# Optimization experiments

Hardware: AMD Instinct MI355X
Metric: run time of the kernel (lower is better)

## Reference

```python
import jax, jax.numpy as jnp
import numpy as np

N_NODES = 50000
N_EDGES = 1600000
IN_FEATS = 256
HIDDEN = 128
N_CLASSES = 40


def setup_inputs() -> dict:
    key = jax.random.key(0)
    k1, k2, k3, k4, k5, k6 = jax.random.split(key, 6)
    inputs = jax.random.normal(k1, (N_NODES, IN_FEATS), dtype=jnp.float32)
    src = jax.random.randint(k2, (N_EDGES,), 0, N_NODES, dtype=jnp.int64 if jax.config.jax_enable_x64 else jnp.int32)
    dst = jax.random.randint(k3, (N_EDGES,), 0, N_NODES, dtype=jnp.int64 if jax.config.jax_enable_x64 else jnp.int32)
    # glorot-style init for GraphConv weights, zero bias (DGL defaults)
    W1 = jax.random.normal(k4, (IN_FEATS, HIDDEN), dtype=jnp.float32) * (1.0 / np.sqrt(IN_FEATS))
    b1 = jnp.zeros((HIDDEN,), dtype=jnp.float32)
    W2 = jax.random.normal(k5, (HIDDEN, N_CLASSES), dtype=jnp.float32) * (1.0 / np.sqrt(HIDDEN))
    b2 = jnp.zeros((N_CLASSES,), dtype=jnp.float32)
    return {"inputs": inputs, "src": src, "dst": dst, "W1": W1, "b1": b1, "W2": W2, "b2": b2}


def _graph_conv(x, W, b, src, dst, deg_out_isqrt, deg_in_isqrt):
    # DGL GraphConv, norm='both': D_dst^{-1/2} A (D_src^{-1/2} X W) + b
    # W applied before aggregation (in_feats >= out_feats path)
    h = (x * deg_out_isqrt[:, None]) @ W                      # [N, out]
    msg = h[src]                                              # [E, out] gather
    agg = jax.ops.segment_sum(msg, dst, num_segments=x.shape[0])  # [N, out] scatter-add
    return agg * deg_in_isqrt[:, None] + b


def reference(inputs, src, dst, W1, b1, W2, b2):
    n = inputs.shape[0]
    ones = jnp.ones((src.shape[0],), dtype=inputs.dtype)
    deg_out = jax.ops.segment_sum(ones, src, num_segments=n)
    deg_in = jax.ops.segment_sum(ones, dst, num_segments=n)
    deg_out_isqrt = jnp.where(deg_out > 0, jax.lax.rsqrt(jnp.maximum(deg_out, 1.0)), 0.0)
    deg_in_isqrt = jnp.where(deg_in > 0, jax.lax.rsqrt(jnp.maximum(deg_in, 1.0)), 0.0)
    h = _graph_conv(inputs, W1, b1, src, dst, deg_out_isqrt, deg_in_isqrt)
    h = _graph_conv(h, W2, b2, src, dst, deg_out_isqrt, deg_in_isqrt)
    return jax.nn.log_softmax(h, axis=1)
```

## Files before the change

### kernel.cpp

```cpp
#include <hip/hip_runtime.h>
#include <math.h>

#define N_NODES 50000
#define N_EDGES 1600000
#define IN_F 256
#define HID 128
#define NCLS 40
#define HS2 40
#define NP 50048
#define NBINS 196
#define MS_BLOCKS 200
#define MS_CHUNK 8000
#define BC_BLOCKS 400
#define BC_CHUNK 4000
#define BIN_CAP 12288

typedef __attribute__((ext_vector_type(8))) short short8;
typedef __attribute__((ext_vector_type(4))) float v4f;
typedef __attribute__((ext_vector_type(2))) _Float16 h2v;

__device__ __forceinline__ unsigned short f2bf(float f) {
    union { float f; unsigned int i; } v;
    v.f = f;
    unsigned int r = v.i + 0x7FFF + ((v.i >> 16) & 1);
    return (unsigned short)(r >> 16);
}
__device__ __forceinline__ h2v u2h(unsigned int u) {
    union { unsigned int i; h2v h; } v; v.i = u; return v.h;
}
__device__ __forceinline__ unsigned int h2u(h2v h) {
    union { h2v h; unsigned int i; } v; v.h = h; return v.i;
}


__global__ __launch_bounds__(256) void k_zero(int* __restrict__ hist_g) {
    for (int i = threadIdx.x; i < 2 * NBINS; i += 256) hist_g[i] = 0;
}


__global__ __launch_bounds__(256) void k_big(const int* __restrict__ src,
                                             const int* __restrict__ dst,
                                             int* __restrict__ hist_g,
                                             const float* __restrict__ W1,
                                             const float* __restrict__ b1,
                                             const float* __restrict__ W2,
                                             short* __restrict__ w12f,
                                             float* __restrict__ b1w2) {
    __shared__ int smem[HID * NCLS];
    int t = threadIdx.x;
    if (blockIdx.x < BC_BLOCKS) {
        int* h = smem;
        for (int i = t; i < 2 * NBINS; i += 256) h[i] = 0;
        __syncthreads();
        int e0 = blockIdx.x * BC_CHUNK;
        for (int i = t * 4; i < BC_CHUNK; i += 1024) {
            int4 d4 = *(const int4*)&dst[e0 + i];
            int4 s4 = *(const int4*)&src[e0 + i];
            atomicAdd(&h[d4.x >> 8], 1);
            atomicAdd(&h[d4.y >> 8], 1);
            atomicAdd(&h[d4.z >> 8], 1);
            atomicAdd(&h[d4.w >> 8], 1);
            atomicAdd(&h[NBINS + (s4.x >> 8)], 1);
            atomicAdd(&h[NBINS + (s4.y >> 8)], 1);
            atomicAdd(&h[NBINS + (s4.z >> 8)], 1);
            atomicAdd(&h[NBINS + (s4.w >> 8)], 1);
        }
        __syncthreads();
        for (int i = t; i < 2 * NBINS; i += 256)
            if (h[i]) atomicAdd(&hist_g[i], h[i]);
        return;
    }
    if (blockIdx.x == BC_BLOCKS + 6) {
        int c = t;
        if (c < NCLS) {
            float a0 = 0.f, a1 = 0.f, a2 = 0.f, a3 = 0.f;
            for (int k = 0; k < HID; k += 4) {
                a0 += b1[k + 0] * W2[(k + 0) * NCLS + c];
                a1 += b1[k + 1] * W2[(k + 1) * NCLS + c];
                a2 += b1[k + 2] * W2[(k + 2) * NCLS + c];
                a3 += b1[k + 3] * W2[(k + 3) * NCLS + c];
            }
            b1w2[c] = (a0 + a1) + (a2 + a3);
        }
        return;
    }
    float* w2s = (float*)smem;
    for (int i = t; i < HID * NCLS; i += 256) w2s[i] = W2[i];
    __syncthreads();
    int g = (blockIdx.x - BC_BLOCKS) * 256 + t;
    int kt = g / 192, rem = g % 192;
    int nt = rem >> 6, lane = rem & 63;
    int q = lane >> 4, n = lane & 15;
    int col = nt * 16 + n;
    float acc[8];
#pragma unroll
    for (int j = 0; j < 8; j++) acc[j] = 0.f;
    if (col < NCLS) {
        int k0 = kt * 32 + q * 8;
        const float* w1r = &W1[(size_t)k0 * HID];
        for (int jj = 0; jj < HID; jj += 4) {
            float w0 = w2s[(jj + 0) * NCLS + col];
            float w1v = w2s[(jj + 1) * NCLS + col];
            float w2v = w2s[(jj + 2) * NCLS + col];
            float w3 = w2s[(jj + 3) * NCLS + col];
#pragma unroll
            for (int j = 0; j < 8; j++) {
                float4 a = *(const float4*)&w1r[j * HID + jj];
                acc[j] += a.x * w0 + a.y * w1v + a.z * w2v + a.w * w3;
            }
        }
    }
    short8 v;
#pragma unroll
    for (int j = 0; j < 8; j++) v[j] = (short)f2bf(acc[j]);
    *(short8*)&w12f[(size_t)g * 8] = v;
}

__global__ __launch_bounds__(256) void k_binscan(const int* __restrict__ hist_g,
                                                 int* __restrict__ bo_d, int* __restrict__ bo_s,
                                                 int* __restrict__ cur_d, int* __restrict__ cur_s) {
    __shared__ int sm[256];
    int t = threadIdx.x;
    for (int side = 0; side < 2; side++) {
        int v = (t < NBINS) ? hist_g[side * NBINS + t] : 0;
        sm[t] = v;
        __syncthreads();
        for (int off = 1; off < 256; off <<= 1) {
            int a = (t >= off) ? sm[t - off] : 0;
            __syncthreads();
            sm[t] += a;
            __syncthreads();
        }
        int ex = sm[t] - v;
        int* bo = side ? bo_s : bo_d;
        int* cu = side ? cur_s : cur_d;
        if (t < NBINS) { bo[t] = ex; cu[t] = ex; }
        if (t == 0) bo[NBINS] = N_EDGES;
        __syncthreads();
    }
}

__global__ __launch_bounds__(256) void k_msscatter(const int* __restrict__ src,
                                                   const int* __restrict__ dst,
                                                   int* __restrict__ cur_d, int* __restrict__ cur_s,
                                                   int* __restrict__ binned_d,
                                                   unsigned char* __restrict__ binned_s) {
    __shared__ int hist[NBINS];
    __shared__ int delta[NBINS];
    __shared__ int lcur[NBINS];
    __shared__ int sm[256];
    __shared__ int stage[MS_CHUNK];
    __shared__ unsigned char binof[MS_CHUNK];
    int t = threadIdx.x;
    int side = blockIdx.x / MS_BLOCKS;
    int e0 = (blockIdx.x % MS_BLOCKS) * MS_CHUNK;
    const int* key = side ? src : dst;
    for (int i = t; i < NBINS; i += 256) hist[i] = 0;
    __syncthreads();
    for (int i = t; i < MS_CHUNK; i += 256) atomicAdd(&hist[key[e0 + i] >> 8], 1);
    __syncthreads();
    int hv = (t < NBINS) ? hist[t] : 0;
    sm[t] = hv;
    __syncthreads();
    for (int off = 1; off < 256; off <<= 1) {
        int a = (t >= off) ? sm[t - off] : 0;
        __syncthreads();
        sm[t] += a;
        __syncthreads();
    }
    if (t < NBINS) {
        int ex = sm[t] - hv;
        int g = atomicAdd(side ? &cur_s[t] : &cur_d[t], hv);
        delta[t] = g - ex;
        lcur[t] = ex;
    }
    __syncthreads();
    if (side == 0) {
        for (int i = t; i < MS_CHUNK; i += 256) {
            int kf = key[e0 + i];
            int v = src[e0 + i];
            int b = kf >> 8;
            int pos = atomicAdd(&lcur[b], 1);
            stage[pos] = ((kf & 255) << 16) | v;
            binof[pos] = (unsigned char)b;
        }
        __syncthreads();
        for (int i = t; i < MS_CHUNK; i += 256)
            binned_d[i + delta[binof[i]]] = stage[i];
    } else {
        for (int i = t; i < MS_CHUNK; i += 256) {
            int kf = key[e0 + i];
            int b = kf >> 8;
            int pos = atomicAdd(&lcur[b], 1);
            stage[pos] = kf & 255;
            binof[pos] = (unsigned char)b;
        }
        __syncthreads();
        for (int i = t; i < MS_CHUNK; i += 256)
            binned_s[i + delta[binof[i]]] = (unsigned char)stage[i];
    }
}

__global__ __launch_bounds__(256) void k_bins(const int* __restrict__ binned_d,
                                              const unsigned char* __restrict__ binned_s,
                                              const int* __restrict__ bo_d, const int* __restrict__ bo_s,
                                              int* __restrict__ offsets, float* __restrict__ din,
                                              float* __restrict__ dout,
                                              unsigned short* __restrict__ csr16) {
    __shared__ int hist[256];
    __shared__ int sm[256];
    __shared__ int cur[256];
    __shared__ int stage[BIN_CAP];
    int t = threadIdx.x;
    hist[t] = 0;
    __syncthreads();
    if (blockIdx.x < NBINS) {
        int bin = blockIdx.x;
        int beg = bo_d[bin], end = bo_d[bin + 1];
        int n = end - beg;
        for (int i = t; i < n; i += 256) atomicAdd(&hist[binned_d[beg + i] >> 16], 1);
        __syncthreads();
        int hv = hist[t];
        sm[t] = hv;
        __syncthreads();
        for (int off = 1; off < 256; off <<= 1) {
            int a = (t >= off) ? sm[t - off] : 0;
            __syncthreads();
            sm[t] += a;
            __syncthreads();
        }
        int ex = sm[t] - hv;
        int node = bin * 256 + t;
        if (node < N_NODES) {
            offsets[node] = beg + ex;
            din[node] = hv ? rsqrtf((float)hv) : 0.f;
        }
        cur[t] = ex;
        __syncthreads();
        for (int i = t; i < n; i += 256) {
            int p = binned_d[beg + i];
            int pos = atomicAdd(&cur[p >> 16], 1);
            if (pos < BIN_CAP) stage[pos] = p & 0xFFFF;
        }
        __syncthreads();
        int m = n < BIN_CAP ? n : BIN_CAP;
        for (int i = t; i < m; i += 256) csr16[beg + i] = (unsigned short)stage[i];
    } else {
        int bin = blockIdx.x - NBINS;
        int beg = bo_s[bin], end = bo_s[bin + 1];
        for (int i = t; i < end - beg; i += 256) atomicAdd(&hist[binned_s[beg + i]], 1);
        __syncthreads();
        int node = bin * 256 + t;
        if (node < N_NODES) {
            int hv2 = hist[t];
            dout[node] = hv2 ? rsqrtf((float)hv2) : 0.f;
        }
    }
}


__global__ __launch_bounds__(256) void k_gemm1(const float* __restrict__ x,
                                               const short* __restrict__ w12f,
                                               const float* __restrict__ dout,
                                               _Float16* __restrict__ gt) {
    int t = threadIdx.x;
    int wv = t >> 6, lane = t & 63;
    int q = lane >> 4, lr = lane & 15;
    int m0 = blockIdx.x * 64 + wv * 16;
    int row = m0 + lr;
    int rowc = min(row, N_NODES - 1);
    v4f acc[3];
#pragma unroll
    for (int n = 0; n < 3; n++) acc[n] = (v4f){0.f, 0.f, 0.f, 0.f};

    const float* xr = &x[(size_t)rowc * IN_F];
#pragma unroll
    for (int kt = 0; kt < 8; kt++) {
        const float4* ap = (const float4*)&xr[kt * 32 + q * 8];
        float4 a0 = ap[0], a1 = ap[1];
        short8 af;
        af[0] = (short)f2bf(a0.x); af[1] = (short)f2bf(a0.y);
        af[2] = (short)f2bf(a0.z); af[3] = (short)f2bf(a0.w);
        af[4] = (short)f2bf(a1.x); af[5] = (short)f2bf(a1.y);
        af[6] = (short)f2bf(a1.z); af[7] = (short)f2bf(a1.w);
#pragma unroll
        for (int nt = 0; nt < 3; nt++) {
            short8 bf = *(const short8*)&w12f[(size_t)((kt * 3 + nt) * 64 + lane) * 8];
            acc[nt] = __builtin_amdgcn_mfma_f32_16x16x32_bf16(af, bf, acc[nt], 0, 0, 0);
        }
    }
    int rbase = m0 + q * 4;
    float4 dv = *(const float4*)&dout[rbase];
#pragma unroll
    for (int i = 0; i < 4; i++) {
        int orow = rbase + i;
        if (orow < N_NODES) {
            float s = (i == 0) ? dv.x : (i == 1) ? dv.y : (i == 2) ? dv.z : dv.w;
#pragma unroll
            for (int nt = 0; nt < 3; nt++) {
                int col = nt * 16 + lr;
                if (col < NCLS)
                    gt[(size_t)orow * HS2 + col] = (_Float16)(acc[nt][i] * s);
            }
        }
    }
}


__global__ __launch_bounds__(256) void k_agg1b(const unsigned short* __restrict__ csr16,
                                               const int* __restrict__ offsets,
                                               const _Float16* __restrict__ g,
                                               const float* __restrict__ din,
                                               const float* __restrict__ dout,
                                               const float* __restrict__ b1w2,
                                               _Float16* __restrict__ h2b) {
    int w = (int)((blockIdx.x * 256 + threadIdx.x) >> 6);
    int wid0 = w * 2;
    if (wid0 >= N_NODES) return;
    int wid1 = wid0 + 1;
    int lane = threadIdx.x & 63;
    int half = lane >> 5;
    int hl = lane & 31;
    int grp = hl >> 3;
    int l = hl & 7;
    bool act = l < 5;
    int colb = min(l, 4) * 8;
    int sbase = half << 5;
    int beg0 = offsets[wid0];
    int beg1 = offsets[wid1];
    int end0 = beg1;
    int end1 = (wid1 + 1 < N_NODES) ? offsets[wid1 + 1] : N_EDGES;
    int myend = half ? end1 : end0;
    h2v a0 = (h2v)0, a1 = (h2v)0, a2 = (h2v)0, a3 = (h2v)0;
    for (int base0 = beg0, base1 = beg1; base0 < end0 || base1 < end1;
         base0 += 32, base1 += 32) {
        int mybase = half ? base1 : base0;
        int idx = mybase + hl;
        int sv = (idx < myend) ? (int)csr16[idx] : 0;
        int mycnt = min(32, myend - mybase);
        int mycl = max(mycnt - 1, 0);
        int e0 = grp * 8 + 0, e1 = grp * 8 + 1, e2 = grp * 8 + 2, e3 = grp * 8 + 3;
        int e4 = grp * 8 + 4, e5 = grp * 8 + 5, e6 = grp * 8 + 6, e7 = grp * 8 + 7;
        int s0 = __shfl(sv, sbase + min(e0, mycl));
        int s1 = __shfl(sv, sbase + min(e1, mycl));
        int s2 = __shfl(sv, sbase + min(e2, mycl));
        int s3 = __shfl(sv, sbase + min(e3, mycl));
        int s4 = __shfl(sv, sbase + min(e4, mycl));
        int s5 = __shfl(sv, sbase + min(e5, mycl));
        int s6 = __shfl(sv, sbase + min(e6, mycl));
        int s7 = __shfl(sv, sbase + min(e7, mycl));
        if (act && mycnt > 0) {
            uint4 v0 = *(const uint4*)&g[(size_t)s0 * HS2 + colb];
            uint4 v1 = *(const uint4*)&g[(size_t)s1 * HS2 + colb];
            uint4 v2 = *(const uint4*)&g[(size_t)s2 * HS2 + colb];
            uint4 v3 = *(const uint4*)&g[(size_t)s3 * HS2 + colb];
            uint4 v4 = *(const uint4*)&g[(size_t)s4 * HS2 + colb];
            uint4 v5 = *(const uint4*)&g[(size_t)s5 * HS2 + colb];
            uint4 v6 = *(const uint4*)&g[(size_t)s6 * HS2 + colb];
            uint4 v7 = *(const uint4*)&g[(size_t)s7 * HS2 + colb];
            if (e0 < mycnt) { a0 += u2h(v0.x); a1 += u2h(v0.y); a2 += u2h(v0.z); a3 += u2h(v0.w); }
            if (e1 < mycnt) { a0 += u2h(v1.x); a1 += u2h(v1.y); a2 += u2h(v1.z); a3 += u2h(v1.w); }
            if (e2 < mycnt) { a0 += u2h(v2.x); a1 += u2h(v2.y); a2 += u2h(v2.z); a3 += u2h(v2.w); }
            if (e3 < mycnt) { a0 += u2h(v3.x); a1 += u2h(v3.y); a2 += u2h(v3.z); a3 += u2h(v3.w); }
            if (e4 < mycnt) { a0 += u2h(v4.x); a1 += u2h(v4.y); a2 += u2h(v4.z); a3 += u2h(v4.w); }
            if (e5 < mycnt) { a0 += u2h(v5.x); a1 += u2h(v5.y); a2 += u2h(v5.z); a3 += u2h(v5.w); }
            if (e6 < mycnt) { a0 += u2h(v6.x); a1 += u2h(v6.y); a2 += u2h(v6.z); a3 += u2h(v6.w); }
            if (e7 < mycnt) { a0 += u2h(v7.x); a1 += u2h(v7.y); a2 += u2h(v7.z); a3 += u2h(v7.w); }
        }
    }
    float c[8];
    c[0] = (float)a0[0]; c[1] = (float)a0[1];
    c[2] = (float)a1[0]; c[3] = (float)a1[1];
    c[4] = (float)a2[0]; c[5] = (float)a2[1];
    c[6] = (float)a3[0]; c[7] = (float)a3[1];
#pragma unroll
    for (int i = 0; i < 8; i++) {
        c[i] += __shfl_xor(c[i], 8);
        c[i] += __shfl_xor(c[i], 16);
    }
    if (grp == 0 && act) {
        int wid = half ? wid1 : wid0;
        float dd = dout[wid];
        float sc = din[wid] * dd;
        float4 bw0 = *(const float4*)&b1w2[colb];
        float4 bw1 = *(const float4*)&b1w2[colb + 4];
        h2v p0, p1, p2, p3;
        p0[0] = (_Float16)(c[0] * sc + bw0.x * dd); p0[1] = (_Float16)(c[1] * sc + bw0.y * dd);
        p1[0] = (_Float16)(c[2] * sc + bw0.z * dd); p1[1] = (_Float16)(c[3] * sc + bw0.w * dd);
        p2[0] = (_Float16)(c[4] * sc + bw1.x * dd); p2[1] = (_Float16)(c[5] * sc + bw1.y * dd);
        p3[0] = (_Float16)(c[6] * sc + bw1.z * dd); p3[1] = (_Float16)(c[7] * sc + bw1.w * dd);
        uint4 o;
        o.x = h2u(p0); o.y = h2u(p1); o.z = h2u(p2); o.w = h2u(p3);
        *(uint4*)&h2b[(size_t)wid * HS2 + colb] = o;
    }
}


__global__ __launch_bounds__(256) void k_agg2(const unsigned short* __restrict__ csr16,
                                              const int* __restrict__ offsets,
                                              const _Float16* __restrict__ h2b,
                                              const float* __restrict__ din,
                                              const float* __restrict__ b2,
                                              float* __restrict__ out) {
    int w = (int)((blockIdx.x * 256 + threadIdx.x) >> 6);
    int wid0 = w * 2;
    if (wid0 >= N_NODES) return;
    int wid1 = wid0 + 1;
    int lane = threadIdx.x & 63;
    int half = lane >> 5;
    int hl = lane & 31;
    int grp = hl >> 3;
    int l = hl & 7;
    bool act = l < 5;
    int colb = min(l, 4) * 8;
    int sbase = half << 5;
    int beg0 = offsets[wid0];
    int beg1 = offsets[wid1];
    int end0 = beg1;
    int end1 = (wid1 + 1 < N_NODES) ? offsets[wid1 + 1] : N_EDGES;
    int myend = half ? end1 : end0;
    h2v a0 = (h2v)0, a1 = (h2v)0, a2 = (h2v)0, a3 = (h2v)0;
    for (int base0 = beg0, base1 = beg1; base0 < end0 || base1 < end1;
         base0 += 32, base1 += 32) {
        int mybase = half ? base1 : base0;
        int idx = mybase + hl;
        int sv = (idx < myend) ? (int)csr16[idx] : 0;
        int mycnt = min(32, myend - mybase);
        int mycl = max(mycnt - 1, 0);
        int e0 = grp * 8 + 0, e1 = grp * 8 + 1, e2 = grp * 8 + 2, e3 = grp * 8 + 3;
        int e4 = grp * 8 + 4, e5 = grp * 8 + 5, e6 = grp * 8 + 6, e7 = grp * 8 + 7;
        int s0 = __shfl(sv, sbase + min(e0, mycl));
        int s1 = __shfl(sv, sbase + min(e1, mycl));
        int s2 = __shfl(sv, sbase + min(e2, mycl));
        int s3 = __shfl(sv, sbase + min(e3, mycl));
        int s4 = __shfl(sv, sbase + min(e4, mycl));
        int s5 = __shfl(sv, sbase + min(e5, mycl));
        int s6 = __shfl(sv, sbase + min(e6, mycl));
        int s7 = __shfl(sv, sbase + min(e7, mycl));
        if (act && mycnt > 0) {
            uint4 v0 = *(const uint4*)&h2b[(size_t)s0 * HS2 + colb];
            uint4 v1 = *(const uint4*)&h2b[(size_t)s1 * HS2 + colb];
            uint4 v2 = *(const uint4*)&h2b[(size_t)s2 * HS2 + colb];
            uint4 v3 = *(const uint4*)&h2b[(size_t)s3 * HS2 + colb];
            uint4 v4 = *(const uint4*)&h2b[(size_t)s4 * HS2 + colb];
            uint4 v5 = *(const uint4*)&h2b[(size_t)s5 * HS2 + colb];
            uint4 v6 = *(const uint4*)&h2b[(size_t)s6 * HS2 + colb];
            uint4 v7 = *(const uint4*)&h2b[(size_t)s7 * HS2 + colb];
            if (e0 < mycnt) { a0 += u2h(v0.x); a1 += u2h(v0.y); a2 += u2h(v0.z); a3 += u2h(v0.w); }
            if (e1 < mycnt) { a0 += u2h(v1.x); a1 += u2h(v1.y); a2 += u2h(v1.z); a3 += u2h(v1.w); }
            if (e2 < mycnt) { a0 += u2h(v2.x); a1 += u2h(v2.y); a2 += u2h(v2.z); a3 += u2h(v2.w); }
            if (e3 < mycnt) { a0 += u2h(v3.x); a1 += u2h(v3.y); a2 += u2h(v3.z); a3 += u2h(v3.w); }
            if (e4 < mycnt) { a0 += u2h(v4.x); a1 += u2h(v4.y); a2 += u2h(v4.z); a3 += u2h(v4.w); }
            if (e5 < mycnt) { a0 += u2h(v5.x); a1 += u2h(v5.y); a2 += u2h(v5.z); a3 += u2h(v5.w); }
            if (e6 < mycnt) { a0 += u2h(v6.x); a1 += u2h(v6.y); a2 += u2h(v6.z); a3 += u2h(v6.w); }
            if (e7 < mycnt) { a0 += u2h(v7.x); a1 += u2h(v7.y); a2 += u2h(v7.z); a3 += u2h(v7.w); }
        }
    }
    float c[8];
    c[0] = (float)a0[0]; c[1] = (float)a0[1];
    c[2] = (float)a1[0]; c[3] = (float)a1[1];
    c[4] = (float)a2[0]; c[5] = (float)a2[1];
    c[6] = (float)a3[0]; c[7] = (float)a3[1];
#pragma unroll
    for (int i = 0; i < 8; i++) {
        c[i] += __shfl_xor(c[i], 8);
        c[i] += __shfl_xor(c[i], 16);
    }
    int wid = half ? wid1 : wid0;
    float sc = din[wid];
    float y[8];
    float lm = -INFINITY;
    if (act) {
        float4 bb0 = *(const float4*)&b2[colb];
        float4 bb1 = *(const float4*)&b2[colb + 4];
        y[0] = c[0] * sc + bb0.x; y[1] = c[1] * sc + bb0.y;
        y[2] = c[2] * sc + bb0.z; y[3] = c[3] * sc + bb0.w;
        y[4] = c[4] * sc + bb1.x; y[5] = c[5] * sc + bb1.y;
        y[6] = c[6] * sc + bb1.z; y[7] = c[7] * sc + bb1.w;
#pragma unroll
        for (int i = 0; i < 8; i++) lm = fmaxf(lm, y[i]);
    }
#pragma unroll
    for (int off = 1; off < 8; off <<= 1) lm = fmaxf(lm, __shfl_xor(lm, off));
    float ls = 0.f;
    if (act) {
#pragma unroll
        for (int i = 0; i < 8; i++) ls += expf(y[i] - lm);
    }
#pragma unroll
    for (int off = 1; off < 8; off <<= 1) ls += __shfl_xor(ls, off);
    if (grp == 0 && act) {
        float lg = logf(ls);
        float4 o0 = make_float4(y[0] - lm - lg, y[1] - lm - lg, y[2] - lm - lg, y[3] - lm - lg);
        float4 o1 = make_float4(y[4] - lm - lg, y[5] - lm - lg, y[6] - lm - lg, y[7] - lm - lg);
        *(float4*)&out[(size_t)wid * NCLS + colb] = o0;
        *(float4*)&out[(size_t)wid * NCLS + colb + 4] = o1;
    }
}


extern "C" void kernel_launch(void* const* d_in, const int* in_sizes, int n_in,
                              void* d_out, int out_size, void* d_ws, size_t ws_size,
                              hipStream_t stream) {
    const float* x  = (const float*)d_in[0];
    const int* src  = (const int*)d_in[1];
    const int* dst  = (const int*)d_in[2];
    const float* W1 = (const float*)d_in[3];
    const float* b1 = (const float*)d_in[4];
    const float* W2 = (const float*)d_in[5];
    const float* b2 = (const float*)d_in[6];
    float* out = (float*)d_out;

    int* wsi   = (int*)d_ws;
    float* wsf = (float*)d_ws;
    int* hist_g   = wsi;
    int* bo_d     = wsi + 512;
    int* bo_s     = wsi + 768;
    int* cur_d    = wsi + 1024;
    int* cur_s    = wsi + 1280;
    float* b1w2   = wsf + 1480;
    int* offsets  = wsi + 1536;
    float* din    = wsf + 1536 + (size_t)NP;
    float* dout   = wsf + 1536 + 2 * (size_t)NP;
    int* binned_d = wsi + 1536 + 3 * (size_t)NP;
    unsigned char* binned_s = (unsigned char*)(binned_d + N_EDGES);
    _Float16* gt  = (_Float16*)(binned_s + N_EDGES);
    _Float16* h2b = gt + (size_t)N_NODES * HS2;
    short* w12f   = (short*)(h2b + (size_t)N_NODES * HS2);
    unsigned short* csr16 = (unsigned short*)(w12f + 12288);

    k_zero<<<1, 256, 0, stream>>>(hist_g);
    k_big<<<BC_BLOCKS + 7, 256, 0, stream>>>(src, dst, hist_g, W1, b1, W2, w12f, b1w2);
    k_binscan<<<1, 256, 0, stream>>>(hist_g, bo_d, bo_s, cur_d, cur_s);
    k_msscatter<<<2 * MS_BLOCKS, 256, 0, stream>>>(src, dst, cur_d, cur_s, binned_d, binned_s);
    k_bins<<<2 * NBINS, 256, 0, stream>>>(binned_d, binned_s, bo_d, bo_s, offsets, din, dout, csr16);
    k_gemm1<<<(N_NODES + 63) / 64, 256, 0, stream>>>(x, w12f, dout, gt);
    k_agg1b<<<(N_NODES / 2) * 64 / 256, 256, 0, stream>>>(csr16, offsets, gt, din, dout, b1w2, h2b);
    k_agg2<<<(N_NODES / 2) * 64 / 256, 256, 0, stream>>>(csr16, offsets, h2b, din, b2, out);
}
```

Measured before the change: 212.7 us.

## Compute out-degrees with direct global atomics instead of binned multisplit

Replaces the source-side binning path (histogram bins, scan, scatter into byte buffer, per-bin counting) with direct global atomicAdd on a per-node degree array during the edge histogram pass. This removes half the multisplit scatter blocks, the source bin scan, and the source half of k_bins, along with the 1.6M-byte binned_s traffic. The cost is 1.6M scattered global atomics into a 50K-entry array, plus zeroing that array in k_zero.

```diff
diff --git a/kernel.cpp b/kernel.cpp
--- a/kernel.cpp
+++ b/kernel.cpp
@@ -33,14 +33,21 @@
 }
 
 
-__global__ __launch_bounds__(256) void k_zero(int* __restrict__ hist_g) {
-    for (int i = threadIdx.x; i < 2 * NBINS; i += 256) hist_g[i] = 0;
+__global__ __launch_bounds__(256) void k_zero(int* __restrict__ hist_g,
+                                              int* __restrict__ deg) {
+    if (blockIdx.x == 196) {
+        for (int i = threadIdx.x; i < NBINS; i += 256) hist_g[i] = 0;
+        return;
+    }
+    int i = blockIdx.x * 256 + threadIdx.x;
+    if (i < NP) deg[i] = 0;
 }
 
 
 __global__ __launch_bounds__(256) void k_big(const int* __restrict__ src,
                                              const int* __restrict__ dst,
                                              int* __restrict__ hist_g,
+                                             int* __restrict__ deg,
                                              const float* __restrict__ W1,
                                              const float* __restrict__ b1,
                                              const float* __restrict__ W2,
@@ -50,7 +57,7 @@
     int t = threadIdx.x;
     if (blockIdx.x < BC_BLOCKS) {
         int* h = smem;
-        for (int i = t; i < 2 * NBINS; i += 256) h[i] = 0;
+        for (int i = t; i < NBINS; i += 256) h[i] = 0;
         __syncthreads();
         int e0 = blockIdx.x * BC_CHUNK;
         for (int i = t * 4; i < BC_CHUNK; i += 1024) {
@@ -60,13 +67,13 @@
             atomicAdd(&h[d4.y >> 8], 1);
             atomicAdd(&h[d4.z >> 8], 1);
             atomicAdd(&h[d4.w >> 8], 1);
-            atomicAdd(&h[NBINS + (s4.x >> 8)], 1);
-            atomicAdd(&h[NBINS + (s4.y >> 8)], 1);
-            atomicAdd(&h[NBINS + (s4.z >> 8)], 1);
-            atomicAdd(&h[NBINS + (s4.w >> 8)], 1);
-        }
-        __syncthreads();
-        for (int i = t; i < 2 * NBINS; i += 256)
+            atomicAdd(&deg[s4.x], 1);
+            atomicAdd(&deg[s4.y], 1);
+            atomicAdd(&deg[s4.z], 1);
+            atomicAdd(&deg[s4.w], 1);
+        }
+        __syncthreads();
+        for (int i = t; i < NBINS; i += 256)
             if (h[i]) atomicAdd(&hist_g[i], h[i]);
         return;
     }
@@ -116,35 +123,31 @@
     *(short8*)&w12f[(size_t)g * 8] = v;
 }
 
+
 __global__ __launch_bounds__(256) void k_binscan(const int* __restrict__ hist_g,
-                                                 int* __restrict__ bo_d, int* __restrict__ bo_s,
-                                                 int* __restrict__ cur_d, int* __restrict__ cur_s) {
+                                                 int* __restrict__ bo_d,
+                                                 int* __restrict__ cur_d) {
     __shared__ int sm[256];
     int t = threadIdx.x;
-    for (int side = 0; side < 2; side++) {
-        int v = (t < NBINS) ? hist_g[side * NBINS + t] : 0;
-        sm[t] = v;
-        __syncthreads();
-        for (int off = 1; off < 256; off <<= 1) {
-            int a = (t >= off) ? sm[t - off] : 0;
-            __syncthreads();
-            sm[t] += a;
-            __syncthreads();
-        }
-        int ex = sm[t] - v;
-        int* bo = side ? bo_s : bo_d;
-        int* cu = side ? cur_s : cur_d;
-        if (t < NBINS) { bo[t] = ex; cu[t] = ex; }
-        if (t == 0) bo[NBINS] = N_EDGES;
-        __syncthreads();
-    }
-}
+    int v = (t < NBINS) ? hist_g[t] : 0;
+    sm[t] = v;
+    __syncthreads();
+    for (int off = 1; off < 256; off <<= 1) {
+        int a = (t >= off) ? sm[t - off] : 0;
+        __syncthreads();
+        sm[t] += a;
+        __syncthreads();
+    }
+    int ex = sm[t] - v;
+    if (t < NBINS) { bo_d[t] = ex; cur_d[t] = ex; }
+    if (t == 0) bo_d[NBINS] = N_EDGES;
+}
+
 
 __global__ __launch_bounds__(256) void k_msscatter(const int* __restrict__ src,
                                                    const int* __restrict__ dst,
-                                                   int* __restrict__ cur_d, int* __restrict__ cur_s,
-                                                   int* __restrict__ binned_d,
-                                                   unsigned char* __restrict__ binned_s) {
+                                                   int* __restrict__ cur_d,
+                                                   int* __restrict__ binned_d) {
     __shared__ int hist[NBINS];
     __shared__ int delta[NBINS];
     __shared__ int lcur[NBINS];
@@ -152,12 +155,10 @@
     __shared__ int stage[MS_CHUNK];
     __shared__ unsigned char binof[MS_CHUNK];
     int t = threadIdx.x;
-    int side = blockIdx.x / MS_BLOCKS;
-    int e0 = (blockIdx.x % MS_BLOCKS) * MS_CHUNK;
-    const int* key = side ? src : dst;
+    int e0 = blockIdx.x * MS_CHUNK;
     for (int i = t; i < NBINS; i += 256) hist[i] = 0;
     __syncthreads();
-    for (int i = t; i < MS_CHUNK; i += 256) atomicAdd(&hist[key[e0 + i] >> 8], 1);
+    for (int i = t; i < MS_CHUNK; i += 256) atomicAdd(&hist[dst[e0 + i] >> 8], 1);
     __syncthreads();
     int hv = (t < NBINS) ? hist[t] : 0;
     sm[t] = hv;
@@ -170,40 +171,28 @@
     }
     if (t < NBINS) {
         int ex = sm[t] - hv;
-        int g = atomicAdd(side ? &cur_s[t] : &cur_d[t], hv);
+        int g = atomicAdd(&cur_d[t], hv);
         delta[t] = g - ex;
         lcur[t] = ex;
     }
     __syncthreads();
-    if (side == 0) {
-        for (int i = t; i < MS_CHUNK; i += 256) {
-            int kf = key[e0 + i];
-            int v = src[e0 + i];
-            int b = kf >> 8;
-            int pos = atomicAdd(&lcur[b], 1);
-            stage[pos] = ((kf & 255) << 16) | v;
-            binof[pos] = (unsigned char)b;
-        }
-        __syncthreads();
-        for (int i = t; i < MS_CHUNK; i += 256)
-            binned_d[i + delta[binof[i]]] = stage[i];
-    } else {
-        for (int i = t; i < MS_CHUNK; i += 256) {
-            int kf = key[e0 + i];
-            int b = kf >> 8;
-            int pos = atomicAdd(&lcur[b], 1);
-            stage[pos] = kf & 255;
-            binof[pos] = (unsigned char)b;
-        }
-        __syncthreads();
-        for (int i = t; i < MS_CHUNK; i += 256)
-            binned_s[i + delta[binof[i]]] = (unsigned char)stage[i];
-    }
-}
+    for (int i = t; i < MS_CHUNK; i += 256) {
+        int kf = dst[e0 + i];
+        int v = src[e0 + i];
+        int b = kf >> 8;
+        int pos = atomicAdd(&lcur[b], 1);
+        stage[pos] = ((kf & 255) << 16) | v;
+        binof[pos] = (unsigned char)b;
+    }
+    __syncthreads();
+    for (int i = t; i < MS_CHUNK; i += 256)
+        binned_d[i + delta[binof[i]]] = stage[i];
+}
+
 
 __global__ __launch_bounds__(256) void k_bins(const int* __restrict__ binned_d,
-                                              const unsigned char* __restrict__ binned_s,
-                                              const int* __restrict__ bo_d, const int* __restrict__ bo_s,
+                                              const int* __restrict__ bo_d,
+                                              const int* __restrict__ deg,
                                               int* __restrict__ offsets, float* __restrict__ din,
                                               float* __restrict__ dout,
                                               unsigned short* __restrict__ csr16) {
@@ -214,48 +203,38 @@
     int t = threadIdx.x;
     hist[t] = 0;
     __syncthreads();
-    if (blockIdx.x < NBINS) {
-        int bin = blockIdx.x;
-        int beg = bo_d[bin], end = bo_d[bin + 1];
-        int n = end - beg;
-        for (int i = t; i < n; i += 256) atomicAdd(&hist[binned_d[beg + i] >> 16], 1);
-        __syncthreads();
-        int hv = hist[t];
-        sm[t] = hv;
-        __syncthreads();
-        for (int off = 1; off < 256; off <<= 1) {
-            int a = (t >= off) ? sm[t - off] : 0;
-            __syncthreads();
-            sm[t] += a;
-            __syncthreads();
-        }
-        int ex = sm[t] - hv;
-        int node = bin * 256 + t;
-        if (node < N_NODES) {
-            offsets[node] = beg + ex;
-            din[node] = hv ? rsqrtf((float)hv) : 0.f;
-        }
-        cur[t] = ex;
-        __syncthreads();
-        for (int i = t; i < n; i += 256) {
-            int p = binned_d[beg + i];
-            int pos = atomicAdd(&cur[p >> 16], 1);
-            if (pos < BIN_CAP) stage[pos] = p & 0xFFFF;
-        }
-        __syncthreads();
-        int m = n < BIN_CAP ? n : BIN_CAP;
-        for (int i = t; i < m; i += 256) csr16[beg + i] = (unsigned short)stage[i];
-    } else {
-        int bin = blockIdx.x - NBINS;
-        int beg = bo_s[bin], end = bo_s[bin + 1];
-        for (int i = t; i < end - beg; i += 256) atomicAdd(&hist[binned_s[beg + i]], 1);
-        __syncthreads();
-        int node = bin * 256 + t;
-        if (node < N_NODES) {
-            int hv2 = hist[t];
-            dout[node] = hv2 ? rsqrtf((float)hv2) : 0.f;
-        }
-    }
+    int bin = blockIdx.x;
+    int beg = bo_d[bin], end = bo_d[bin + 1];
+    int n = end - beg;
+    for (int i = t; i < n; i += 256) atomicAdd(&hist[binned_d[beg + i] >> 16], 1);
+    __syncthreads();
+    int hv = hist[t];
+    sm[t] = hv;
+    __syncthreads();
+    for (int off = 1; off < 256; off <<= 1) {
+        int a = (t >= off) ? sm[t - off] : 0;
+        __syncthreads();
+        sm[t] += a;
+        __syncthreads();
+    }
+    int ex = sm[t] - hv;
+    int node = bin * 256 + t;
+    if (node < N_NODES) {
+        offsets[node] = beg + ex;
+        din[node] = hv ? rsqrtf((float)hv) : 0.f;
+        int dv = deg[node];
+        dout[node] = dv ? rsqrtf((float)dv) : 0.f;
+    }
+    cur[t] = ex;
+    __syncthreads();
+    for (int i = t; i < n; i += 256) {
+        int p = binned_d[beg + i];
+        int pos = atomicAdd(&cur[p >> 16], 1);
+        if (pos < BIN_CAP) stage[pos] = p & 0xFFFF;
+    }
+    __syncthreads();
+    int m = n < BIN_CAP ? n : BIN_CAP;
+    for (int i = t; i < m; i += 256) csr16[beg + i] = (unsigned short)stage[i];
 }
 
 
@@ -515,25 +494,23 @@
     float* wsf = (float*)d_ws;
     int* hist_g   = wsi;
     int* bo_d     = wsi + 512;
-    int* bo_s     = wsi + 768;
     int* cur_d    = wsi + 1024;
-    int* cur_s    = wsi + 1280;
     float* b1w2   = wsf + 1480;
     int* offsets  = wsi + 1536;
     float* din    = wsf + 1536 + (size_t)NP;
     float* dout   = wsf + 1536 + 2 * (size_t)NP;
-    int* binned_d = wsi + 1536 + 3 * (size_t)NP;
-    unsigned char* binned_s = (unsigned char*)(binned_d + N_EDGES);
-    _Float16* gt  = (_Float16*)(binned_s + N_EDGES);
+    int* deg      = wsi + 1536 + 3 * (size_t)NP;
+    int* binned_d = wsi + 1536 + 4 * (size_t)NP;
+    _Float16* gt  = (_Float16*)(binned_d + N_EDGES);
     _Float16* h2b = gt + (size_t)N_NODES * HS2;
     short* w12f   = (short*)(h2b + (size_t)N_NODES * HS2);
     unsigned short* csr16 = (unsigned short*)(w12f + 12288);
 
-    k_zero<<<1, 256, 0, stream>>>(hist_g);
-    k_big<<<BC_BLOCKS + 7, 256, 0, stream>>>(src, dst, hist_g, W1, b1, W2, w12f, b1w2);
-    k_binscan<<<1, 256, 0, stream>>>(hist_g, bo_d, bo_s, cur_d, cur_s);
-    k_msscatter<<<2 * MS_BLOCKS, 256, 0, stream>>>(src, dst, cur_d, cur_s, binned_d, binned_s);
-    k_bins<<<2 * NBINS, 256, 0, stream>>>(binned_d, binned_s, bo_d, bo_s, offsets, din, dout, csr16);
+    k_zero<<<197, 256, 0, stream>>>(hist_g, deg);
+    k_big<<<BC_BLOCKS + 7, 256, 0, stream>>>(src, dst, hist_g, deg, W1, b1, W2, w12f, b1w2);
+    k_binscan<<<1, 256, 0, stream>>>(hist_g, bo_d, cur_d);
+    k_msscatter<<<MS_BLOCKS, 256, 0, stream>>>(src, dst, cur_d, binned_d);
+    k_bins<<<NBINS, 256, 0, stream>>>(binned_d, bo_d, deg, offsets, din, dout, csr16);
     k_gemm1<<<(N_NODES + 63) / 64, 256, 0, stream>>>(x, w12f, dout, gt);
     k_agg1b<<<(N_NODES / 2) * 64 / 256, 256, 0, stream>>>(csr16, offsets, gt, din, dout, b1w2, h2b);
     k_agg2<<<(N_NODES / 2) * 64 / 256, 256, 0, stream>>>(csr16, offsets, h2b, din, b2, out);
```

Result: slower. 272.6 us (+28.2%).

## Replace histogram-and-scan binning with fixed-capacity bins and fuse weight precompute

Applied to the files above, without the earlier changes.

Drops the global histogram pass, the bin scan kernel and the zeroing kernel. Each bin now gets a fixed region of BIN_CAP slots, so the multi-split scatter appends with per-bin atomic cursors initialized to bin*BIN_CAP, and the W1·W2 precompute blocks run inside the same kernel. Because CSR segments are no longer contiguous, a per-node 16-bit degree array is added and the aggregation kernels use offset plus degree to find segment ends. This removes two launches and one full read of src/dst, but bins with more than BIN_CAP edges would overflow, and the binned buffers grow.

```diff
diff --git a/kernel.cpp b/kernel.cpp
--- a/kernel.cpp
+++ b/kernel.cpp
@@ -11,8 +11,6 @@
 #define NBINS 196
 #define MS_BLOCKS 200
 #define MS_CHUNK 8000
-#define BC_BLOCKS 400
-#define BC_CHUNK 4000
 #define BIN_CAP 12288
 
 typedef __attribute__((ext_vector_type(8))) short short8;
@@ -33,44 +31,85 @@
 }
 
 
-__global__ __launch_bounds__(256) void k_zero(int* __restrict__ hist_g) {
-    for (int i = threadIdx.x; i < 2 * NBINS; i += 256) hist_g[i] = 0;
-}
-
-
-__global__ __launch_bounds__(256) void k_big(const int* __restrict__ src,
-                                             const int* __restrict__ dst,
-                                             int* __restrict__ hist_g,
-                                             const float* __restrict__ W1,
-                                             const float* __restrict__ b1,
-                                             const float* __restrict__ W2,
-                                             short* __restrict__ w12f,
-                                             float* __restrict__ b1w2) {
-    __shared__ int smem[HID * NCLS];
+__global__ __launch_bounds__(256) void k_init(int* __restrict__ cur_d,
+                                              int* __restrict__ cur_s) {
     int t = threadIdx.x;
-    if (blockIdx.x < BC_BLOCKS) {
-        int* h = smem;
-        for (int i = t; i < 2 * NBINS; i += 256) h[i] = 0;
-        __syncthreads();
-        int e0 = blockIdx.x * BC_CHUNK;
-        for (int i = t * 4; i < BC_CHUNK; i += 1024) {
-            int4 d4 = *(const int4*)&dst[e0 + i];
-            int4 s4 = *(const int4*)&src[e0 + i];
-            atomicAdd(&h[d4.x >> 8], 1);
-            atomicAdd(&h[d4.y >> 8], 1);
-            atomicAdd(&h[d4.z >> 8], 1);
-            atomicAdd(&h[d4.w >> 8], 1);
-            atomicAdd(&h[NBINS + (s4.x >> 8)], 1);
-            atomicAdd(&h[NBINS + (s4.y >> 8)], 1);
-            atomicAdd(&h[NBINS + (s4.z >> 8)], 1);
-            atomicAdd(&h[NBINS + (s4.w >> 8)], 1);
-        }
-        __syncthreads();
-        for (int i = t; i < 2 * NBINS; i += 256)
-            if (h[i]) atomicAdd(&hist_g[i], h[i]);
+    if (t < NBINS) {
+        cur_d[t] = t * BIN_CAP;
+        cur_s[t] = t * BIN_CAP;
+    }
+}
+
+
+__global__ __launch_bounds__(256) void k_ms(const int* __restrict__ src,
+                                            const int* __restrict__ dst,
+                                            int* __restrict__ cur_d, int* __restrict__ cur_s,
+                                            int* __restrict__ binned_d,
+                                            unsigned char* __restrict__ binned_s,
+                                            const float* __restrict__ W1,
+                                            const float* __restrict__ b1,
+                                            const float* __restrict__ W2,
+                                            short* __restrict__ w12f,
+                                            float* __restrict__ b1w2) {
+    __shared__ int smem[11024];
+    int t = threadIdx.x;
+    if (blockIdx.x < 2 * MS_BLOCKS) {
+        int* hist  = smem;
+        int* delta = smem + 256;
+        int* lcur  = smem + 512;
+        int* sm    = smem + 768;
+        int* stage = smem + 1024;
+        unsigned char* binof = (unsigned char*)(smem + 9024);
+        int side = blockIdx.x / MS_BLOCKS;
+        int e0 = (blockIdx.x % MS_BLOCKS) * MS_CHUNK;
+        const int* key = side ? src : dst;
+        for (int i = t; i < NBINS; i += 256) hist[i] = 0;
+        __syncthreads();
+        for (int i = t; i < MS_CHUNK; i += 256) atomicAdd(&hist[key[e0 + i] >> 8], 1);
+        __syncthreads();
+        int hv = (t < NBINS) ? hist[t] : 0;
+        sm[t] = hv;
+        __syncthreads();
+        for (int off = 1; off < 256; off <<= 1) {
+            int a = (t >= off) ? sm[t - off] : 0;
+            __syncthreads();
+            sm[t] += a;
+            __syncthreads();
+        }
+        if (t < NBINS) {
+            int ex = sm[t] - hv;
+            int g = atomicAdd(side ? &cur_s[t] : &cur_d[t], hv);
+            delta[t] = g - ex;
+            lcur[t] = ex;
+        }
+        __syncthreads();
+        if (side == 0) {
+            for (int i = t; i < MS_CHUNK; i += 256) {
+                int kf = key[e0 + i];
+                int v = src[e0 + i];
+                int b = kf >> 8;
+                int pos = atomicAdd(&lcur[b], 1);
+                stage[pos] = ((kf & 255) << 16) | v;
+                binof[pos] = (unsigned char)b;
+            }
+            __syncthreads();
+            for (int i = t; i < MS_CHUNK; i += 256)
+                binned_d[i + delta[binof[i]]] = stage[i];
+        } else {
+            for (int i = t; i < MS_CHUNK; i += 256) {
+                int kf = key[e0 + i];
+                int b = kf >> 8;
+                int pos = atomicAdd(&lcur[b], 1);
+                stage[pos] = kf & 255;
+                binof[pos] = (unsigned char)b;
+            }
+            __syncthreads();
+            for (int i = t; i < MS_CHUNK; i += 256)
+                binned_s[i + delta[binof[i]]] = (unsigned char)stage[i];
+        }
         return;
     }
-    if (blockIdx.x == BC_BLOCKS + 6) {
+    if (blockIdx.x == 2 * MS_BLOCKS + 6) {
         int c = t;
         if (c < NCLS) {
             float a0 = 0.f, a1 = 0.f, a2 = 0.f, a3 = 0.f;
@@ -87,7 +126,7 @@
     float* w2s = (float*)smem;
     for (int i = t; i < HID * NCLS; i += 256) w2s[i] = W2[i];
     __syncthreads();
-    int g = (blockIdx.x - BC_BLOCKS) * 256 + t;
+    int g = (blockIdx.x - 2 * MS_BLOCKS) * 256 + t;
     int kt = g / 192, rem = g % 192;
     int nt = rem >> 6, lane = rem & 63;
     int q = lane >> 4, n = lane & 15;
@@ -116,96 +155,14 @@
     *(short8*)&w12f[(size_t)g * 8] = v;
 }
 
-__global__ __launch_bounds__(256) void k_binscan(const int* __restrict__ hist_g,
-                                                 int* __restrict__ bo_d, int* __restrict__ bo_s,
-                                                 int* __restrict__ cur_d, int* __restrict__ cur_s) {
-    __shared__ int sm[256];
-    int t = threadIdx.x;
-    for (int side = 0; side < 2; side++) {
-        int v = (t < NBINS) ? hist_g[side * NBINS + t] : 0;
-        sm[t] = v;
-        __syncthreads();
-        for (int off = 1; off < 256; off <<= 1) {
-            int a = (t >= off) ? sm[t - off] : 0;
-            __syncthreads();
-            sm[t] += a;
-            __syncthreads();
-        }
-        int ex = sm[t] - v;
-        int* bo = side ? bo_s : bo_d;
-        int* cu = side ? cur_s : cur_d;
-        if (t < NBINS) { bo[t] = ex; cu[t] = ex; }
-        if (t == 0) bo[NBINS] = N_EDGES;
-        __syncthreads();
-    }
-}
-
-__global__ __launch_bounds__(256) void k_msscatter(const int* __restrict__ src,
-                                                   const int* __restrict__ dst,
-                                                   int* __restrict__ cur_d, int* __restrict__ cur_s,
-                                                   int* __restrict__ binned_d,
-                                                   unsigned char* __restrict__ binned_s) {
-    __shared__ int hist[NBINS];
-    __shared__ int delta[NBINS];
-    __shared__ int lcur[NBINS];
-    __shared__ int sm[256];
-    __shared__ int stage[MS_CHUNK];
-    __shared__ unsigned char binof[MS_CHUNK];
-    int t = threadIdx.x;
-    int side = blockIdx.x / MS_BLOCKS;
-    int e0 = (blockIdx.x % MS_BLOCKS) * MS_CHUNK;
-    const int* key = side ? src : dst;
-    for (int i = t; i < NBINS; i += 256) hist[i] = 0;
-    __syncthreads();
-    for (int i = t; i < MS_CHUNK; i += 256) atomicAdd(&hist[key[e0 + i] >> 8], 1);
-    __syncthreads();
-    int hv = (t < NBINS) ? hist[t] : 0;
-    sm[t] = hv;
-    __syncthreads();
-    for (int off = 1; off < 256; off <<= 1) {
-        int a = (t >= off) ? sm[t - off] : 0;
-        __syncthreads();
-        sm[t] += a;
-        __syncthreads();
-    }
-    if (t < NBINS) {
-        int ex = sm[t] - hv;
-        int g = atomicAdd(side ? &cur_s[t] : &cur_d[t], hv);
-        delta[t] = g - ex;
-        lcur[t] = ex;
-    }
-    __syncthreads();
-    if (side == 0) {
-        for (int i = t; i < MS_CHUNK; i += 256) {
-            int kf = key[e0 + i];
-            int v = src[e0 + i];
-            int b = kf >> 8;
-            int pos = atomicAdd(&lcur[b], 1);
-            stage[pos] = ((kf & 255) << 16) | v;
-            binof[pos] = (unsigned char)b;
-        }
-        __syncthreads();
-        for (int i = t; i < MS_CHUNK; i += 256)
-            binned_d[i + delta[binof[i]]] = stage[i];
-    } else {
-        for (int i = t; i < MS_CHUNK; i += 256) {
-            int kf = key[e0 + i];
-            int b = kf >> 8;
-            int pos = atomicAdd(&lcur[b], 1);
-            stage[pos] = kf & 255;
-            binof[pos] = (unsigned char)b;
-        }
-        __syncthreads();
-        for (int i = t; i < MS_CHUNK; i += 256)
-            binned_s[i + delta[binof[i]]] = (unsigned char)stage[i];
-    }
-}
 
 __global__ __launch_bounds__(256) void k_bins(const int* __restrict__ binned_d,
                                               const unsigned char* __restrict__ binned_s,
-                                              const int* __restrict__ bo_d, const int* __restrict__ bo_s,
+                                              const int* __restrict__ cur_d,
+                                              const int* __restrict__ cur_s,
                                               int* __restrict__ offsets, float* __restrict__ din,
                                               float* __restrict__ dout,
+                                              unsigned short* __restrict__ deg16,
                                               unsigned short* __restrict__ csr16) {
     __shared__ int hist[256];
     __shared__ int sm[256];
@@ -216,8 +173,8 @@
     __syncthreads();
     if (blockIdx.x < NBINS) {
         int bin = blockIdx.x;
-        int beg = bo_d[bin], end = bo_d[bin + 1];
-        int n = end - beg;
+        int beg = bin * BIN_CAP;
+        int n = cur_d[bin] - beg;
         for (int i = t; i < n; i += 256) atomicAdd(&hist[binned_d[beg + i] >> 16], 1);
         __syncthreads();
         int hv = hist[t];
@@ -233,6 +190,7 @@
         int node = bin * 256 + t;
         if (node < N_NODES) {
             offsets[node] = beg + ex;
+            deg16[node] = (unsigned short)hv;
             din[node] = hv ? rsqrtf((float)hv) : 0.f;
         }
         cur[t] = ex;
@@ -247,8 +205,9 @@
         for (int i = t; i < m; i += 256) csr16[beg + i] = (unsigned short)stage[i];
     } else {
         int bin = blockIdx.x - NBINS;
-        int beg = bo_s[bin], end = bo_s[bin + 1];
-        for (int i = t; i < end - beg; i += 256) atomicAdd(&hist[binned_s[beg + i]], 1);
+        int beg = bin * BIN_CAP;
+        int n = cur_s[bin] - beg;
+        for (int i = t; i < n; i += 256) atomicAdd(&hist[binned_s[beg + i]], 1);
         __syncthreads();
         int node = bin * 256 + t;
         if (node < N_NODES) {
@@ -309,6 +268,7 @@
 
 __global__ __launch_bounds__(256) void k_agg1b(const unsigned short* __restrict__ csr16,
                                                const int* __restrict__ offsets,
+                                               const unsigned short* __restrict__ deg16,
                                                const _Float16* __restrict__ g,
                                                const float* __restrict__ din,
                                                const float* __restrict__ dout,
@@ -328,8 +288,9 @@
     int sbase = half << 5;
     int beg0 = offsets[wid0];
     int beg1 = offsets[wid1];
-    int end0 = beg1;
-    int end1 = (wid1 + 1 < N_NODES) ? offsets[wid1 + 1] : N_EDGES;
+    unsigned int dp = *(const unsigned int*)&deg16[wid0];
+    int end0 = beg0 + (int)(dp & 0xFFFFu);
+    int end1 = beg1 + (int)(dp >> 16);
     int myend = half ? end1 : end0;
     h2v a0 = (h2v)0, a1 = (h2v)0, a2 = (h2v)0, a3 = (h2v)0;
     for (int base0 = beg0, base1 = beg1; base0 < end0 || base1 < end1;
@@ -398,6 +359,7 @@
 
 __global__ __launch_bounds__(256) void k_agg2(const unsigned short* __restrict__ csr16,
                                               const int* __restrict__ offsets,
+                                              const unsigned short* __restrict__ deg16,
                                               const _Float16* __restrict__ h2b,
                                               const float* __restrict__ din,
                                               const float* __restrict__ b2,
@@ -416,8 +378,9 @@
     int sbase = half << 5;
     int beg0 = offsets[wid0];
     int beg1 = offsets[wid1];
-    int end0 = beg1;
-    int end1 = (wid1 + 1 < N_NODES) ? offsets[wid1 + 1] : N_EDGES;
+    unsigned int dp = *(const unsigned int*)&deg16[wid0];
+    int end0 = beg0 + (int)(dp & 0xFFFFu);
+    int end1 = beg1 + (int)(dp >> 16);
     int myend = half ? end1 : end0;
     h2v a0 = (h2v)0, a1 = (h2v)0, a2 = (h2v)0, a3 = (h2v)0;
     for (int base0 = beg0, base1 = beg1; base0 < end0 || base1 < end1;
@@ -513,28 +476,27 @@
 
     int* wsi   = (int*)d_ws;
     float* wsf = (float*)d_ws;
-    int* hist_g   = wsi;
-    int* bo_d     = wsi + 512;
-    int* bo_s     = wsi + 768;
-    int* cur_d    = wsi + 1024;
-    int* cur_s    = wsi + 1280;
-    float* b1w2   = wsf + 1480;
+    const size_t BINREG = (size_t)NBINS * BIN_CAP;
+    int* cur_d    = wsi;
+    int* cur_s    = wsi + 256;
+    float* b1w2   = wsf + 512;
     int* offsets  = wsi + 1536;
     float* din    = wsf + 1536 + (size_t)NP;
     float* dout   = wsf + 1536 + 2 * (size_t)NP;
-    int* binned_d = wsi + 1536 + 3 * (size_t)NP;
-    unsigned char* binned_s = (unsigned char*)(binned_d + N_EDGES);
-    _Float16* gt  = (_Float16*)(binned_s + N_EDGES);
+    unsigned short* deg16 = (unsigned short*)(wsi + 1536 + 3 * (size_t)NP);
+    int* binned_d = wsi + 1536 + 3 * (size_t)NP + NP / 2;
+    unsigned char* binned_s = (unsigned char*)(binned_d + BINREG);
+    _Float16* gt  = (_Float16*)(binned_s + BINREG);
     _Float16* h2b = gt + (size_t)N_NODES * HS2;
     short* w12f   = (short*)(h2b + (size_t)N_NODES * HS2);
     unsigned short* csr16 = (unsigned short*)(w12f + 12288);
 
-    k_zero<<<1, 256, 0, stream>>>(hist_g);
-    k_big<<<BC_BLOCKS + 7, 256, 0, stream>>>(src, dst, hist_g, W1, b1, W2, w12f, b1w2);
-    k_binscan<<<1, 256, 0, stream>>>(hist_g, bo_d, bo_s, cur_d, cur_s);
-    k_msscatter<<<2 * MS_BLOCKS, 256, 0, stream>>>(src, dst, cur_d, cur_s, binned_d, binned_s);
-    k_bins<<<2 * NBINS, 256, 0, stream>>>(binned_d, binned_s, bo_d, bo_s, offsets, din, dout, csr16);
+    k_init<<<1, 256, 0, stream>>>(cur_d, cur_s);
+    k_ms<<<2 * MS_BLOCKS + 7, 256, 0, stream>>>(src, dst, cur_d, cur_s, binned_d, binned_s,
+                                                W1, b1, W2, w12f, b1w2);
+    k_bins<<<2 * NBINS, 256, 0, stream>>>(binned_d, binned_s, cur_d, cur_s,
+                                          offsets, din, dout, deg16, csr16);
     k_gemm1<<<(N_NODES + 63) / 64, 256, 0, stream>>>(x, w12f, dout, gt);
-    k_agg1b<<<(N_NODES / 2) * 64 / 256, 256, 0, stream>>>(csr16, offsets, gt, din, dout, b1w2, h2b);
-    k_agg2<<<(N_NODES / 2) * 64 / 256, 256, 0, stream>>>(csr16, offsets, h2b, din, b2, out);
-}
+    k_agg1b<<<(N_NODES / 2) * 64 / 256, 256, 0, stream>>>(csr16, offsets, deg16, gt, din, dout, b1w2, h2b);
+    k_agg2<<<(N_NODES / 2) * 64 / 256, 256, 0, stream>>>(csr16, offsets, deg16, h2b, din, b2, out);
+}
```

Result: faster. 193.1 us (median of 2 runs) (-9.2%).
